# Performance work log

Hardware: AMD Instinct MI355X
Metric: run time of the kernel (lower is better)

Reference implementation:

```python
import jax, jax.numpy as jnp
import numpy as np

B, N, D, E = 8, 2048, 2048, 64
CAP = 64


def setup_inputs() -> dict:
    key = jax.random.key(0)
    k1, k2 = jax.random.split(key)
    token_inputs = jax.random.normal(k1, (B, N, D), dtype=jnp.float32)
    w_gate = jax.random.normal(k2, (D, E), dtype=jnp.float32)
    return {"token_inputs": token_inputs, "w_gate": w_gate, "expert_capacity": CAP}


def reference(token_inputs, w_gate, expert_capacity):
    # gate projection: [b,n,d] x [d,e] -> [b,n,e]
    router_logits = jnp.einsum('bnd,de->bne', token_inputs, w_gate)
    # router z-loss: mean over tokens of logsumexp(logits)^2
    z = jax.nn.logsumexp(router_logits, axis=-1)
    router_z_loss = jnp.mean(z * z)
    router_probs = jax.nn.softmax(router_logits, axis=-1)
    num_experts = router_probs.shape[-1]
    # top-1 expert per token (Switch routing)
    expert_gate = jnp.max(router_probs, axis=-1)           # [b,n]
    expert_index = jnp.argmax(router_probs, axis=-1)       # [b,n]
    expert_mask = jax.nn.one_hot(expert_index, num_experts, dtype=router_probs.dtype)  # [b,n,e]
    # position of each token within its chosen expert's buffer (0-based);
    # -1 where the token did not pick that expert
    position_in_expert = jnp.cumsum(expert_mask, axis=1) * expert_mask - 1.0  # [b,n,e]
    # one_hot zeroes out positions < 0 or >= capacity (capacity overflow drop)
    dispatch_mask = jax.nn.one_hot(position_in_expert.astype(jnp.int32),
                                   expert_capacity, dtype=router_probs.dtype)  # [b,n,e,c]
    combine_array = dispatch_mask * expert_gate[..., None, None]               # [b,n,e,c]
    return dispatch_mask, combine_array, router_z_loss
```

## Files before the change

### kernel.cpp

```cpp
#include <hip/hip_runtime.h>
#include <cstdint>
#include <cstddef>

#define B_ 8
#define N_ 2048
#define D_ 2048
#define E_ 64
#define CAP_ 64
#define NTOK (B_*N_)
#define GEMM_BLOCKS 256
#define FILL_BLOCKS 4096
#define DC 64
#define NTILE (D_/DC)
#define MASK_ELEMS ((size_t)NTOK*(size_t)E_*(size_t)CAP_)

typedef float f32x4 __attribute__((ext_vector_type(4)));
typedef short bf16x8 __attribute__((ext_vector_type(8)));
typedef unsigned int u32;
typedef u32 u32x2 __attribute__((ext_vector_type(2)));

__device__ __forceinline__ u32 f2bf(float f) {
  u32 u = __float_as_uint(f);
  return (u + 0x7fffu + ((u >> 16) & 1u)) >> 16;
}
__device__ __forceinline__ float bf2f(u32 b) { return __uint_as_float(b << 16); }

__global__ __launch_bounds__(256)
void k_wconv(const float* __restrict__ W, u32* __restrict__ whi, u32* __restrict__ wlo) {
  const int i = blockIdx.x * 256 + threadIdx.x;
  const int g = i & 7, e = (i >> 3) & 63, t = i >> 9;
  const int d0 = t * DC + g * 8;
  const int dst = ((t * 64 + e) * 8 + (g ^ (e & 7))) * 4;
  #pragma unroll
  for (int jj = 0; jj < 4; ++jj) {
    const float x0 = W[(size_t)(d0 + 2*jj    ) * E_ + e];
    const float x1 = W[(size_t)(d0 + 2*jj + 1) * E_ + e];
    const u32 h0 = f2bf(x0), h1 = f2bf(x1);
    const u32 l0 = f2bf(x0 - bf2f(h0)), l1 = f2bf(x1 - bf2f(h1));
    whi[dst + jj] = h0 | (h1 << 16);
    wlo[dst + jj] = l0 | (l1 << 16);
  }
}

__global__ __launch_bounds__(256)
void k_gemm_zero(const float* __restrict__ X, const u32* __restrict__ whi,
                 const u32* __restrict__ wlo, float* __restrict__ out,
                 float* __restrict__ gate_ws, int* __restrict__ idx_ws,
                 float* __restrict__ z_ws) {
  const int bid = blockIdx.x;
  if (bid >= GEMM_BLOCKS) {
    const int zb   = bid - GEMM_BLOCKS;
    const int tid  = threadIdx.x;
    const int wid  = tid >> 6, lane = tid & 63;
    const f32x4 z4 = {0.f, 0.f, 0.f, 0.f};
    f32x4* p = (f32x4*)out + ((size_t)zb*8192 + wid*256 + lane);
    #pragma unroll
    for (int j = 0; j < 8; ++j) {
      __builtin_nontemporal_store(z4, p +   0);
      __builtin_nontemporal_store(z4, p +  64);
      __builtin_nontemporal_store(z4, p + 128);
      __builtin_nontemporal_store(z4, p + 192);
      p += 1024;
    }
    if (zb == 0 && tid == 0) out[2*MASK_ELEMS] = 0.f;
    return;
  }

  __shared__ __align__(16) char lds[2][32768];
  const int tid  = threadIdx.x;
  const int lane = tid & 63;
  const int wid  = __builtin_amdgcn_readfirstlane(tid >> 6);
  const int tokbase = bid * 64;
  const int woff = wid * 16;
  const int rA = lane & 15, kg = lane >> 4;

  int xr_r[4], xr_q[4], xw_off[4];
  #pragma unroll
  for (int p = 0; p < 4; ++p) {
    const int c = p*256 + tid;
    const int r = c >> 4, q = c & 15;
    xr_r[p] = r; xr_q[p] = q;
    xw_off[p] = r*128 + (((q >> 1) ^ (r & 7)) << 4) + ((q & 1) << 3);
  }
  const f32x4* xg   = (const f32x4*)X;
  const f32x4* whi4 = (const f32x4*)whi;
  const f32x4* wlo4 = (const f32x4*)wlo;

  f32x4 xr[4], wr[4];

#define XW_LOAD(t)                                                            \
  { _Pragma("unroll")                                                         \
    for (int p = 0; p < 4; ++p)                                               \
      xr[p] = xg[(size_t)(tokbase + xr_r[p])*512 + (size_t)(t)*16 + xr_q[p]]; \
    wr[0] = whi4[(size_t)(t)*512 + tid];                                      \
    wr[1] = whi4[(size_t)(t)*512 + 256 + tid];                                \
    wr[2] = wlo4[(size_t)(t)*512 + tid];                                      \
    wr[3] = wlo4[(size_t)(t)*512 + 256 + tid]; }

#define XW_STORE(buf)                                                         \
  { char* bq = lds[buf];                                                      \
    _Pragma("unroll")                                                         \
    for (int p = 0; p < 4; ++p) {                                             \
      const u32 h0 = f2bf(xr[p][0]), h1 = f2bf(xr[p][1]);                     \
      const u32 h2 = f2bf(xr[p][2]), h3 = f2bf(xr[p][3]);                     \
      const u32 l0 = f2bf(xr[p][0] - bf2f(h0)), l1 = f2bf(xr[p][1] - bf2f(h1)); \
      const u32 l2 = f2bf(xr[p][2] - bf2f(h2)), l3 = f2bf(xr[p][3] - bf2f(h3)); \
      u32x2 hp; hp[0] = h0 | (h1 << 16); hp[1] = h2 | (h3 << 16);             \
      u32x2 lp; lp[0] = l0 | (l1 << 16); lp[1] = l2 | (l3 << 16);             \
      *(u32x2*)(bq + xw_off[p])        = hp;                                  \
      *(u32x2*)(bq + 8192 + xw_off[p]) = lp;                                  \
    }                                                                         \
    *(f32x4*)(bq + 16384 +        tid*16) = wr[0];                            \
    *(f32x4*)(bq + 16384 + 4096 + tid*16) = wr[1];                            \
    *(f32x4*)(bq + 24576 +        tid*16) = wr[2];                            \
    *(f32x4*)(bq + 24576 + 4096 + tid*16) = wr[3]; }

  XW_LOAD(0);
  XW_STORE(0);
  __syncthreads();

  f32x4 acc[4];
  #pragma unroll
  for (int eb = 0; eb < 4; ++eb) { acc[eb][0]=0.f; acc[eb][1]=0.f; acc[eb][2]=0.f; acc[eb][3]=0.f; }

  const int tokrow = woff + rA;
  for (int t = 0; t < NTILE; ++t) {
    if (t + 1 < NTILE) XW_LOAD(t + 1);

    const char* bp = lds[t & 1];
    #pragma unroll
    for (int kk = 0; kk < 2; ++kk) {
      const int gA = ((kk*4 + kg) ^ (rA & 7)) << 4;
      const bf16x8 Ah = *(const bf16x8*)(bp +        tokrow*128 + gA);
      const bf16x8 Al = *(const bf16x8*)(bp + 8192 + tokrow*128 + gA);
      #pragma unroll
      for (int eb = 0; eb < 4; ++eb) {
        const int e  = eb*16 + rA;
        const int gB = ((kk*4 + kg) ^ (e & 7)) << 4;
        const bf16x8 Bh = *(const bf16x8*)(bp + 16384 + e*128 + gB);
        const bf16x8 Bl = *(const bf16x8*)(bp + 24576 + e*128 + gB);
        acc[eb] = __builtin_amdgcn_mfma_f32_16x16x32_bf16(Ah, Bh, acc[eb], 0, 0, 0);
        acc[eb] = __builtin_amdgcn_mfma_f32_16x16x32_bf16(Ah, Bl, acc[eb], 0, 0, 0);
        acc[eb] = __builtin_amdgcn_mfma_f32_16x16x32_bf16(Al, Bh, acc[eb], 0, 0, 0);
        acc[eb] = __builtin_amdgcn_mfma_f32_16x16x32_bf16(Al, Bl, acc[eb], 0, 0, 0);
      }
    }

    if (t + 1 < NTILE) XW_STORE((t + 1) & 1);
    __syncthreads();
  }

  float* Lg = (float*)&lds[0][0];
  #pragma unroll
  for (int eb = 0; eb < 4; ++eb)
    #pragma unroll
    for (int r = 0; r < 4; ++r)
      Lg[(woff + kg*4 + r)*65 + eb*16 + rA] = acc[eb][r];
  __syncthreads();

  #pragma unroll 1
  for (int i = 0; i < 16; ++i) {
    const int tkn = woff + i;
    const float v = Lg[tkn*65 + lane];
    float vmax = v; int vidx = lane;
    #pragma unroll
    for (int m = 1; m < 64; m <<= 1) {
      const float om = __shfl_xor(vmax, m);
      const int   oi = __shfl_xor(vidx, m);
      if (om > vmax || (om == vmax && oi < vidx)) { vmax = om; vidx = oi; }
    }
    float se = expf(v - vmax);
    #pragma unroll
    for (int m = 1; m < 64; m <<= 1) se += __shfl_xor(se, m);
    if (lane == 0) {
      const int row = tokbase + tkn;
      gate_ws[row] = 1.0f / se;
      idx_ws[row]  = vidx;
      z_ws[row]    = vmax + logf(se);
    }
  }
#undef XW_LOAD
#undef XW_STORE
}

__global__ __launch_bounds__(64)
void k_route(const float* __restrict__ gate_ws, const int* __restrict__ idx_ws,
             const float* __restrict__ z_ws, float* __restrict__ out) {
  const int b    = blockIdx.x;
  const int lane = threadIdx.x;
  float* dispatch = out;
  float* combine  = out + MASK_ELEMS;

  int   cnt  = 0;
  float zsum = 0.f;
  const unsigned long long below = (1ULL << lane) - 1ULL;

  for (int n0 = 0; n0 < N_; n0 += 64) {
    const int   t    = b*N_ + n0 + lane;
    const int   idx  = idx_ws[t];
    const float gate = gate_ws[t];
    const float z    = z_ws[t];
    zsum += z * z;

    unsigned long long bb[6];
    #pragma unroll
    for (int k = 0; k < 6; ++k) bb[k] = __ballot((idx >> k) & 1);

    unsigned long long m_tok = ~0ULL, m_exp = ~0ULL;
    #pragma unroll
    for (int k = 0; k < 6; ++k) {
      m_tok &= ((idx  >> k) & 1) ? bb[k] : ~bb[k];
      m_exp &= ((lane >> k) & 1) ? bb[k] : ~bb[k];
    }

    const int rank = __popcll(m_tok & below);
    const int base = __shfl(cnt, idx);
    const int pos  = base + rank;
    cnt += __popcll(m_exp);

    if (pos < CAP_) {
      const size_t o = (((size_t)t)*E_ + (size_t)idx)*CAP_ + (size_t)pos;
      dispatch[o] = 1.0f;
      combine[o]  = gate;
    }
  }

  #pragma unroll
  for (int m = 1; m < 64; m <<= 1) zsum += __shfl_xor(zsum, m);
  if (lane == 0) atomicAdd(out + 2*MASK_ELEMS, zsum * (1.0f / (float)NTOK));
}

extern "C" void kernel_launch(void* const* d_in, const int* in_sizes, int n_in,
                              void* d_out, int out_size, void* d_ws, size_t ws_size,
                              hipStream_t stream) {
  const float* X = (const float*)d_in[0];
  const float* W = (const float*)d_in[1];
  float* out = (float*)d_out;

  char* wsb = (char*)d_ws;
  u32*   whi     = (u32*)  (wsb);
  u32*   wlo     = (u32*)  (wsb + 262144);
  float* gate_ws = (float*)(wsb + 524288);
  int*   idx_ws  = (int*)  (wsb + 589824);
  float* z_ws    = (float*)(wsb + 655360);

  hipLaunchKernelGGL(k_wconv, dim3(64), dim3(256), 0, stream, W, whi, wlo);
  hipLaunchKernelGGL(k_gemm_zero, dim3(GEMM_BLOCKS + FILL_BLOCKS), dim3(256), 0, stream,
                     X, whi, wlo, out, gate_ws, idx_ws, z_ws);
  hipLaunchKernelGGL(k_route, dim3(B_), dim3(64), 0, stream,
                     gate_ws, idx_ws, z_ws, out);
}
```

Baseline: 141.6 us.

## Load gate weights directly from global into MFMA registers, halve LDS

```diff
diff --git a/kernel.cpp b/kernel.cpp
--- a/kernel.cpp
+++ b/kernel.cpp
@@ -10,6 +10,7 @@
 #define NTOK (B_*N_)
 #define GEMM_BLOCKS 256
 #define FILL_BLOCKS 4096
+#define TOTAL_BLOCKS (GEMM_BLOCKS + FILL_BLOCKS)
 #define DC 64
 #define NTILE (D_/DC)
 #define MASK_ELEMS ((size_t)NTOK*(size_t)E_*(size_t)CAP_)
@@ -30,7 +31,7 @@
   const int i = blockIdx.x * 256 + threadIdx.x;
   const int g = i & 7, e = (i >> 3) & 63, t = i >> 9;
   const int d0 = t * DC + g * 8;
-  const int dst = ((t * 64 + e) * 8 + (g ^ (e & 7))) * 4;
+  const int dst = i * 4;
   #pragma unroll
   for (int jj = 0; jj < 4; ++jj) {
     const float x0 = W[(size_t)(d0 + 2*jj    ) * E_ + e];
@@ -66,7 +67,7 @@
     return;
   }
 
-  __shared__ __align__(16) char lds[2][32768];
+  __shared__ __align__(16) char lds[2][16384];
   const int tid  = threadIdx.x;
   const int lane = tid & 63;
   const int wid  = __builtin_amdgcn_readfirstlane(tid >> 6);
@@ -82,20 +83,16 @@
     xr_r[p] = r; xr_q[p] = q;
     xw_off[p] = r*128 + (((q >> 1) ^ (r & 7)) << 4) + ((q & 1) << 3);
   }
-  const f32x4* xg   = (const f32x4*)X;
-  const f32x4* whi4 = (const f32x4*)whi;
-  const f32x4* wlo4 = (const f32x4*)wlo;
-
-  f32x4 xr[4], wr[4];
+  const f32x4* xg = (const f32x4*)X;
+  const bf16x8* wh8 = (const bf16x8*)whi;
+  const bf16x8* wl8 = (const bf16x8*)wlo;
+
+  f32x4 xr[4];
 
 #define XW_LOAD(t)                                                            \
   { _Pragma("unroll")                                                         \
     for (int p = 0; p < 4; ++p)                                               \
-      xr[p] = xg[(size_t)(tokbase + xr_r[p])*512 + (size_t)(t)*16 + xr_q[p]]; \
-    wr[0] = whi4[(size_t)(t)*512 + tid];                                      \
-    wr[1] = whi4[(size_t)(t)*512 + 256 + tid];                                \
-    wr[2] = wlo4[(size_t)(t)*512 + tid];                                      \
-    wr[3] = wlo4[(size_t)(t)*512 + 256 + tid]; }
+      xr[p] = xg[(size_t)(tokbase + xr_r[p])*512 + (size_t)(t)*16 + xr_q[p]]; }
 
 #define XW_STORE(buf)                                                         \
   { char* bq = lds[buf];                                                      \
@@ -109,11 +106,7 @@
       u32x2 lp; lp[0] = l0 | (l1 << 16); lp[1] = l2 | (l3 << 16);             \
       *(u32x2*)(bq + xw_off[p])        = hp;                                  \
       *(u32x2*)(bq + 8192 + xw_off[p]) = lp;                                  \
-    }                                                                         \
-    *(f32x4*)(bq + 16384 +        tid*16) = wr[0];                            \
-    *(f32x4*)(bq + 16384 + 4096 + tid*16) = wr[1];                            \
-    *(f32x4*)(bq + 24576 +        tid*16) = wr[2];                            \
-    *(f32x4*)(bq + 24576 + 4096 + tid*16) = wr[3]; }
+    } }
 
   XW_LOAD(0);
   XW_STORE(0);
@@ -124,8 +117,20 @@
   for (int eb = 0; eb < 4; ++eb) { acc[eb][0]=0.f; acc[eb][1]=0.f; acc[eb][2]=0.f; acc[eb][3]=0.f; }
 
   const int tokrow = woff + rA;
+  const int wlane = rA*8 + kg;
+
   for (int t = 0; t < NTILE; ++t) {
     if (t + 1 < NTILE) XW_LOAD(t + 1);
+
+    bf16x8 Bh[2][4], Bl[2][4];
+    #pragma unroll
+    for (int kk = 0; kk < 2; ++kk)
+      #pragma unroll
+      for (int eb = 0; eb < 4; ++eb) {
+        const int gi = t*512 + eb*128 + wlane + kk*4;
+        Bh[kk][eb] = wh8[gi];
+        Bl[kk][eb] = wl8[gi];
+      }
 
     const char* bp = lds[t & 1];
     #pragma unroll
@@ -135,14 +140,10 @@
       const bf16x8 Al = *(const bf16x8*)(bp + 8192 + tokrow*128 + gA);
       #pragma unroll
       for (int eb = 0; eb < 4; ++eb) {
-        const int e  = eb*16 + rA;
-        const int gB = ((kk*4 + kg) ^ (e & 7)) << 4;
-        const bf16x8 Bh = *(const bf16x8*)(bp + 16384 + e*128 + gB);
-        const bf16x8 Bl = *(const bf16x8*)(bp + 24576 + e*128 + gB);
-        acc[eb] = __builtin_amdgcn_mfma_f32_16x16x32_bf16(Ah, Bh, acc[eb], 0, 0, 0);
-        acc[eb] = __builtin_amdgcn_mfma_f32_16x16x32_bf16(Ah, Bl, acc[eb], 0, 0, 0);
-        acc[eb] = __builtin_amdgcn_mfma_f32_16x16x32_bf16(Al, Bh, acc[eb], 0, 0, 0);
-        acc[eb] = __builtin_amdgcn_mfma_f32_16x16x32_bf16(Al, Bl, acc[eb], 0, 0, 0);
+        acc[eb] = __builtin_amdgcn_mfma_f32_16x16x32_bf16(Ah, Bh[kk][eb], acc[eb], 0, 0, 0);
+        acc[eb] = __builtin_amdgcn_mfma_f32_16x16x32_bf16(Ah, Bl[kk][eb], acc[eb], 0, 0, 0);
+        acc[eb] = __builtin_amdgcn_mfma_f32_16x16x32_bf16(Al, Bh[kk][eb], acc[eb], 0, 0, 0);
+        acc[eb] = __builtin_amdgcn_mfma_f32_16x16x32_bf16(Al, Bl[kk][eb], acc[eb], 0, 0, 0);
       }
     }
 
@@ -150,7 +151,7 @@
     __syncthreads();
   }
 
-  float* Lg = (float*)&lds[0][0];
+  float* Lg = (float*)lds;
   #pragma unroll
   for (int eb = 0; eb < 4; ++eb)
     #pragma unroll
@@ -245,7 +246,7 @@
   float* z_ws    = (float*)(wsb + 655360);
 
   hipLaunchKernelGGL(k_wconv, dim3(64), dim3(256), 0, stream, W, whi, wlo);
-  hipLaunchKernelGGL(k_gemm_zero, dim3(GEMM_BLOCKS + FILL_BLOCKS), dim3(256), 0, stream,
+  hipLaunchKernelGGL(k_gemm_zero, dim3(TOTAL_BLOCKS), dim3(256), 0, stream,
                      X, whi, wlo, out, gate_ws, idx_ws, z_ws);
   hipLaunchKernelGGL(k_route, dim3(B_), dim3(64), 0, stream,
                      gate_ws, idx_ws, z_ws, out);
```

New measurement: 182.5 us. 1.29x slower.

## Move output zero-fill into the weight-conversion kernel, separating it from the GEMM

Applied to the files above, without the earlier changes.

```diff
diff --git a/kernel.cpp b/kernel.cpp
--- a/kernel.cpp
+++ b/kernel.cpp
@@ -9,6 +9,7 @@
 #define CAP_ 64
 #define NTOK (B_*N_)
 #define GEMM_BLOCKS 256
+#define WCONV_BLOCKS 64
 #define FILL_BLOCKS 4096
 #define DC 64
 #define NTILE (D_/DC)
@@ -26,46 +27,46 @@
 __device__ __forceinline__ float bf2f(u32 b) { return __uint_as_float(b << 16); }
 
 __global__ __launch_bounds__(256)
-void k_wconv(const float* __restrict__ W, u32* __restrict__ whi, u32* __restrict__ wlo) {
-  const int i = blockIdx.x * 256 + threadIdx.x;
-  const int g = i & 7, e = (i >> 3) & 63, t = i >> 9;
-  const int d0 = t * DC + g * 8;
-  const int dst = ((t * 64 + e) * 8 + (g ^ (e & 7))) * 4;
-  #pragma unroll
-  for (int jj = 0; jj < 4; ++jj) {
-    const float x0 = W[(size_t)(d0 + 2*jj    ) * E_ + e];
-    const float x1 = W[(size_t)(d0 + 2*jj + 1) * E_ + e];
-    const u32 h0 = f2bf(x0), h1 = f2bf(x1);
-    const u32 l0 = f2bf(x0 - bf2f(h0)), l1 = f2bf(x1 - bf2f(h1));
-    whi[dst + jj] = h0 | (h1 << 16);
-    wlo[dst + jj] = l0 | (l1 << 16);
-  }
+void k_fill_wconv(const float* __restrict__ W, u32* __restrict__ whi,
+                  u32* __restrict__ wlo, float* __restrict__ out) {
+  const int bid = blockIdx.x;
+  const int tid = threadIdx.x;
+  if (bid < WCONV_BLOCKS) {
+    const int i = bid * 256 + tid;
+    const int g = i & 7, e = (i >> 3) & 63, t = i >> 9;
+    const int d0 = t * DC + g * 8;
+    const int dst = ((t * 64 + e) * 8 + (g ^ (e & 7))) * 4;
+    #pragma unroll
+    for (int jj = 0; jj < 4; ++jj) {
+      const float x0 = W[(size_t)(d0 + 2*jj    ) * E_ + e];
+      const float x1 = W[(size_t)(d0 + 2*jj + 1) * E_ + e];
+      const u32 h0 = f2bf(x0), h1 = f2bf(x1);
+      const u32 l0 = f2bf(x0 - bf2f(h0)), l1 = f2bf(x1 - bf2f(h1));
+      whi[dst + jj] = h0 | (h1 << 16);
+      wlo[dst + jj] = l0 | (l1 << 16);
+    }
+    return;
+  }
+  const int zb   = bid - WCONV_BLOCKS;
+  const int wid  = tid >> 6, lane = tid & 63;
+  const f32x4 z4 = {0.f, 0.f, 0.f, 0.f};
+  f32x4* p = (f32x4*)out + ((size_t)zb*8192 + wid*256 + lane);
+  #pragma unroll
+  for (int j = 0; j < 8; ++j) {
+    p[  0] = z4;
+    p[ 64] = z4;
+    p[128] = z4;
+    p[192] = z4;
+    p += 1024;
+  }
+  if (zb == 0 && tid == 0) out[2*MASK_ELEMS] = 0.f;
 }
 
 __global__ __launch_bounds__(256)
-void k_gemm_zero(const float* __restrict__ X, const u32* __restrict__ whi,
-                 const u32* __restrict__ wlo, float* __restrict__ out,
-                 float* __restrict__ gate_ws, int* __restrict__ idx_ws,
-                 float* __restrict__ z_ws) {
+void k_gemm(const float* __restrict__ X, const u32* __restrict__ whi,
+            const u32* __restrict__ wlo, float* __restrict__ gate_ws,
+            int* __restrict__ idx_ws, float* __restrict__ z_ws) {
   const int bid = blockIdx.x;
-  if (bid >= GEMM_BLOCKS) {
-    const int zb   = bid - GEMM_BLOCKS;
-    const int tid  = threadIdx.x;
-    const int wid  = tid >> 6, lane = tid & 63;
-    const f32x4 z4 = {0.f, 0.f, 0.f, 0.f};
-    f32x4* p = (f32x4*)out + ((size_t)zb*8192 + wid*256 + lane);
-    #pragma unroll
-    for (int j = 0; j < 8; ++j) {
-      __builtin_nontemporal_store(z4, p +   0);
-      __builtin_nontemporal_store(z4, p +  64);
-      __builtin_nontemporal_store(z4, p + 128);
-      __builtin_nontemporal_store(z4, p + 192);
-      p += 1024;
-    }
-    if (zb == 0 && tid == 0) out[2*MASK_ELEMS] = 0.f;
-    return;
-  }
-
   __shared__ __align__(16) char lds[2][32768];
   const int tid  = threadIdx.x;
   const int lane = tid & 63;
@@ -244,9 +245,10 @@
   int*   idx_ws  = (int*)  (wsb + 589824);
   float* z_ws    = (float*)(wsb + 655360);
 
-  hipLaunchKernelGGL(k_wconv, dim3(64), dim3(256), 0, stream, W, whi, wlo);
-  hipLaunchKernelGGL(k_gemm_zero, dim3(GEMM_BLOCKS + FILL_BLOCKS), dim3(256), 0, stream,
-                     X, whi, wlo, out, gate_ws, idx_ws, z_ws);
+  hipLaunchKernelGGL(k_fill_wconv, dim3(WCONV_BLOCKS + FILL_BLOCKS), dim3(256), 0, stream,
+                     W, whi, wlo, out);
+  hipLaunchKernelGGL(k_gemm, dim3(GEMM_BLOCKS), dim3(256), 0, stream,
+                     X, whi, wlo, gate_ws, idx_ws, z_ws);
   hipLaunchKernelGGL(k_route, dim3(B_), dim3(64), 0, stream,
                      gate_ws, idx_ws, z_ws, out);
 }
```

Measured after the change: 198.6 us. 1.4x slower.
